# Performance work log

Hardware: AMD Instinct MI355X
Metric: run time of the kernel (lower is better)

The kernel has to match this reference:

```python
import jax, jax.numpy as jnp
import numpy as np

N = 100_000          # nodes
E = 3_200_000        # edges
DIM = 64             # filt_conv_dimension
L = 3                # filt_conv_number
MAX_DEG = 64         # embedding table size = MAX_DEG + 1
SUM_DIMS = DIM * (L + 1)  # 256, fc input
BN_EPS = 1e-5
NEG_SLOPE = 0.01


def _leaky(x):
    return jnp.where(x >= 0, x, NEG_SLOPE * x)


def _batchnorm(x, g, b):
    # training-mode BN over the node axis
    mu = jnp.mean(x, axis=0, keepdims=True)
    var = jnp.var(x, axis=0, keepdims=True)
    return g * (x - mu) * jax.lax.rsqrt(var + BN_EPS) + b


def setup_inputs() -> dict:
    key = jax.random.key(0)
    ks = jax.random.split(key, 16)
    s = 0.05
    inp = {
        "node_deg": jax.random.randint(ks[0], (N,), 0, MAX_DEG, dtype=jnp.int32),
        "edge_index": jax.random.randint(ks[1], (2, E), 0, N, dtype=jnp.int32),
        "embed_deg": jax.random.normal(ks[2], (MAX_DEG + 1, DIM), jnp.float32) * s,
        "eps": jnp.zeros((L,), jnp.float32),
        "W1": jax.random.normal(ks[3], (L, DIM, DIM), jnp.float32) * s,
        "b1": jnp.zeros((L, DIM), jnp.float32),
        "W2": jax.random.normal(ks[4], (L, DIM, DIM), jnp.float32) * s,
        "b2": jnp.zeros((L, DIM), jnp.float32),
        "bn_g": jnp.ones((L, DIM), jnp.float32),
        "bn_b": jnp.zeros((L, DIM), jnp.float32),
        "fc_W1": jax.random.normal(ks[5], (SUM_DIMS, DIM), jnp.float32) * s,
        "fc_b1": jnp.zeros((DIM,), jnp.float32),
        "fc_bn_g": jnp.ones((DIM,), jnp.float32),
        "fc_bn_b": jnp.zeros((DIM,), jnp.float32),
        "fc_W2": jax.random.normal(ks[6], (DIM, 1), jnp.float32) * s,
        "fc_b2": jnp.zeros((1,), jnp.float32),
    }
    return inp


def reference(node_deg, edge_index, embed_deg, eps, W1, b1, W2, b2,
              bn_g, bn_b, fc_W1, fc_b1, fc_bn_g, fc_bn_b, fc_W2, fc_b2):
    src, dst = edge_index[0], edge_index[1]
    h = embed_deg[node_deg]                       # [N, DIM]
    z = [h]
    for l in range(L):
        x = z[-1]
        # GINConv: (1+eps)*x_i + sum_{j->i} x_j, then MLP lin_lrelu_lin
        agg = jax.ops.segment_sum(x[src], dst, num_segments=N)  # [N, DIM]
        m = (1.0 + eps[l]) * x + agg
        h1 = _leaky(m @ W1[l] + b1[l])
        out = h1 @ W2[l] + b2[l]
        out = _leaky(_batchnorm(out, bn_g[l], bn_b[l]))
        z.append(out)
    xcat = jnp.concatenate(z, axis=1)             # [N, SUM_DIMS]
    hfc = _leaky(_batchnorm(xcat @ fc_W1 + fc_b1, fc_bn_g, fc_bn_b))
    ret = jax.nn.sigmoid(hfc @ fc_W2 + fc_b2)     # [N, 1]
    return jnp.squeeze(ret, axis=-1)              # [N]
```

## Files before the change

### kernel.cpp

```cpp
#include <hip/hip_runtime.h>
#include <hip/hip_bf16.h>

#define NN 100000
#define NE 3200000
#define D 64
#define BN_EPS 1e-5f

#define NP 512
#define CHUNK 6250
#define NB 391
#define SPREAD 16

typedef float v2f __attribute__((ext_vector_type(2)));

#define FMA4(accr, xs, w4) \
  accr.x += (xs) * (w4).x; accr.y += (xs) * (w4).y; \
  accr.z += (xs) * (w4).z; accr.w += (xs) * (w4).w;

__global__ __launch_bounds__(256) void bucket_kernel(const int* __restrict__ ei,
    const int* __restrict__ deg, int* __restrict__ rec, int* __restrict__ S) {
  __shared__ int cntL[392];
  __shared__ int curL[392];
  __shared__ int scanbuf[256];
  int t = threadIdx.x;
  int p = blockIdx.x;
  int e0 = p * CHUNK;
  cntL[t] = 0;
  if (t < 136) cntL[256 + t] = 0;
  __syncthreads();
  {
    int e = t;
    for (; e + 768 < CHUNK; e += 1024) {
      int d0 = ei[NE + e0 + e];
      int d1 = ei[NE + e0 + e + 256];
      int d2 = ei[NE + e0 + e + 512];
      int d3 = ei[NE + e0 + e + 768];
      atomicAdd(&cntL[(unsigned)d0 >> 8], 1);
      atomicAdd(&cntL[(unsigned)d1 >> 8], 1);
      atomicAdd(&cntL[(unsigned)d2 >> 8], 1);
      atomicAdd(&cntL[(unsigned)d3 >> 8], 1);
    }
    for (; e < CHUNK; e += 256) {
      int dd = ei[NE + e0 + e];
      atomicAdd(&cntL[(unsigned)dd >> 8], 1);
    }
  }
  __syncthreads();
  int a0 = 0, a1 = 0;
  if (t < 196) { a0 = cntL[2 * t]; a1 = cntL[2 * t + 1]; }
  int s = a0 + a1;
  scanbuf[t] = s;
  __syncthreads();
  for (int off = 1; off < 256; off <<= 1) {
    int x = (t >= off) ? scanbuf[t - off] : 0;
    __syncthreads();
    scanbuf[t] += x;
    __syncthreads();
  }
  int ex = scanbuf[t] - s;
  if (t < 196) {
    curL[2 * t]     = ex;
    curL[2 * t + 1] = ex + a0;
    S[p * 392 + 2 * t]     = e0 + ex;
    S[p * 392 + 2 * t + 1] = e0 + ex + a0;
  }
  __syncthreads();
  {
    int e = t;
    for (; e + 768 < CHUNK; e += 1024) {
      int s0 = ei[e0 + e],       d0 = ei[NE + e0 + e];
      int s1 = ei[e0 + e + 256], d1 = ei[NE + e0 + e + 256];
      int s2 = ei[e0 + e + 512], d2 = ei[NE + e0 + e + 512];
      int s3 = ei[e0 + e + 768], d3 = ei[NE + e0 + e + 768];
      int g0 = deg[s0], g1 = deg[s1], g2 = deg[s2], g3 = deg[s3];
      int p0 = atomicAdd(&curL[(unsigned)d0 >> 8], 1);
      int p1 = atomicAdd(&curL[(unsigned)d1 >> 8], 1);
      int p2 = atomicAdd(&curL[(unsigned)d2 >> 8], 1);
      int p3 = atomicAdd(&curL[(unsigned)d3 >> 8], 1);
      rec[e0 + p0] = s0 | ((d0 & 255) << 17) | (g0 << 25);
      rec[e0 + p1] = s1 | ((d1 & 255) << 17) | (g1 << 25);
      rec[e0 + p2] = s2 | ((d2 & 255) << 17) | (g2 << 25);
      rec[e0 + p3] = s3 | ((d3 & 255) << 17) | (g3 << 25);
    }
    for (; e < CHUNK; e += 256) {
      int ss = ei[e0 + e];
      int dd = ei[NE + e0 + e];
      int dg = deg[ss];
      int b = (unsigned)dd >> 8;
      int pos = atomicAdd(&curL[b], 1);
      rec[e0 + pos] = ss | ((dd & 255) << 17) | (dg << 25);
    }
  }
}

__global__ __launch_bounds__(256) void bucketsum_kernel(const int* __restrict__ S,
    int* __restrict__ bsum) {
  __shared__ int sh[256];
  int B = blockIdx.x;
  int t = threadIdx.x;
  int c = 0;
  for (int p = t; p < NP; p += 256)
    c += S[p * 392 + B + 1] - S[p * 392 + B];
  sh[t] = c;
  __syncthreads();
  for (int o = 128; o > 0; o >>= 1) {
    if (t < o) sh[t] += sh[t + o];
    __syncthreads();
  }
  if (t == 0) bsum[B] = sh[0];
}

__global__ __launch_bounds__(512) void scan2_kernel(int* __restrict__ bsum) {
  __shared__ int sh[512];
  int t = threadIdx.x;
  int v = (t < NB) ? bsum[t] : 0;
  sh[t] = v;
  __syncthreads();
  for (int o = 1; o < 512; o <<= 1) {
    int x = (t >= o) ? sh[t - o] : 0;
    __syncthreads();
    sh[t] += x;
    __syncthreads();
  }
  if (t < NB) bsum[t] = sh[t] - v;
}

__global__ __launch_bounds__(512) void sort_kernel(const int* __restrict__ rec,
    const int* __restrict__ S, const int* __restrict__ bsum,
    int* __restrict__ csroff, int* __restrict__ csrsrc,
    unsigned* __restrict__ cnt8) {
  __shared__ int cntL[256];
  __shared__ int curL[256];
  __shared__ unsigned hist[256 * 33];
  int t = threadIdx.x;
  int B = blockIdx.x;
  if (t < 256) cntL[t] = 0;
  for (int k = t; k < 256 * 33; k += 512) hist[k] = 0;
  __syncthreads();
  int lane = t & 15;
  int g = t >> 4;
  for (int p = g; p < NP; p += 32) {
    int s0 = S[p * 392 + B], s1 = S[p * 392 + B + 1];
    for (int e = s0 + lane; e < s1; e += 16) {
      int r = rec[e];
      int dl = (r >> 17) & 255;
      int dg = (unsigned)r >> 25;
      atomicAdd(&cntL[dl], 1);
      atomicAdd(&hist[dl * 33 + (dg >> 1)], (dg & 1) ? 0x10000u : 1u);
    }
  }
  __syncthreads();
  int v = 0;
  if (t < 256) { v = cntL[t]; curL[t] = v; }
  __syncthreads();
  for (int o = 1; o < 256; o <<= 1) {
    int x = 0;
    if (t < 256 && t >= o) x = curL[t - o];
    __syncthreads();
    if (t < 256) curL[t] += x;
    __syncthreads();
  }
  int b0 = bsum[B];
  if (t < 256) {
    int excl = curL[t] - v;
    int node = B * 256 + t;
    if (node <= NN) csroff[node] = b0 + excl;
  }
  __syncthreads();
  if (t < 256) curL[t] = b0 + (curL[t] - v);
  if (t < 256) {
    int node = B * 256 + t;
    if (node < NN) {
      #pragma unroll
      for (int j = 0; j < 16; j++) {
        unsigned p0 = hist[t * 33 + 2 * j];
        unsigned p1 = hist[t * 33 + 2 * j + 1];
        unsigned p = (p0 & 255) | (((p0 >> 16) & 255) << 8)
                   | ((p1 & 255) << 16) | (((p1 >> 16) & 255) << 24);
        cnt8[(long)node * 16 + j] = p;
      }
    }
  }
  __syncthreads();
  for (int p = g; p < NP; p += 32) {
    int s0 = S[p * 392 + B], s1 = S[p * 392 + B + 1];
    for (int e = s0 + lane; e < s1; e += 16) {
      int r = rec[e];
      int pos = atomicAdd(&curL[(r >> 17) & 255], 1);
      csrsrc[pos] = r & 0x1FFFF;
    }
  }
}

__global__ __launch_bounds__(256) void agg_kernel(const int* __restrict__ off,
    const int* __restrict__ srcs, const unsigned* __restrict__ xh32,
    float* __restrict__ agg) {
  int t = threadIdx.x;
  int lane = t & 15;
  int g = t >> 4;
  int i = blockIdx.x * 16 + g;
  int e0 = off[i], e1 = off[i + 1];
  float s0 = 0.f, s1 = 0.f, s2 = 0.f, s3 = 0.f;
  int e = e0;
  for (; e + 4 <= e1; e += 4) {
    int j0 = srcs[e + 0], j1 = srcs[e + 1], j2 = srcs[e + 2], j3 = srcs[e + 3];
    unsigned u0 = xh32[(long)j0 * 16 + lane];
    unsigned u1 = xh32[(long)j1 * 16 + lane];
    unsigned u2 = xh32[(long)j2 * 16 + lane];
    unsigned u3 = xh32[(long)j3 * 16 + lane];
    v2f l0 = __builtin_amdgcn_cvt_pk_f32_fp8((int)u0, false);
    v2f h0 = __builtin_amdgcn_cvt_pk_f32_fp8((int)u0, true);
    v2f l1 = __builtin_amdgcn_cvt_pk_f32_fp8((int)u1, false);
    v2f h1 = __builtin_amdgcn_cvt_pk_f32_fp8((int)u1, true);
    v2f l2 = __builtin_amdgcn_cvt_pk_f32_fp8((int)u2, false);
    v2f h2 = __builtin_amdgcn_cvt_pk_f32_fp8((int)u2, true);
    v2f l3 = __builtin_amdgcn_cvt_pk_f32_fp8((int)u3, false);
    v2f h3 = __builtin_amdgcn_cvt_pk_f32_fp8((int)u3, true);
    s0 += (l0.x + l1.x) + (l2.x + l3.x);
    s1 += (l0.y + l1.y) + (l2.y + l3.y);
    s2 += (h0.x + h1.x) + (h2.x + h3.x);
    s3 += (h0.y + h1.y) + (h2.y + h3.y);
  }
  for (; e < e1; e++) {
    unsigned u = xh32[(long)srcs[e] * 16 + lane];
    v2f lo = __builtin_amdgcn_cvt_pk_f32_fp8((int)u, false);
    v2f hi = __builtin_amdgcn_cvt_pk_f32_fp8((int)u, true);
    s0 += lo.x; s1 += lo.y; s2 += hi.x; s3 += hi.y;
  }
  *(float4*)&agg[(long)i * D + lane * 4] = make_float4(s0, s1, s2, s3);
}

__global__ __launch_bounds__(256) void layer_kernel(
    const float* __restrict__ X,
    const float* __restrict__ AGG,
    const unsigned* __restrict__ CNT8, const float* __restrict__ EMB,
    const int* __restrict__ deg, float* __restrict__ Z0,
    const float* __restrict__ epsv, int l,
    const float* __restrict__ W1, const float* __restrict__ b1,
    const float* __restrict__ W2, const float* __restrict__ b2,
    float* __restrict__ Z, float* __restrict__ spread)
{
  __shared__ float Ws[64][64];
  __shared__ float XsT[64][64];
  int t = threadIdx.x;
  int i0 = blockIdx.x * 64;
  float alpha = 1.0f + epsv[l];
  int c0 = (t & 15) * 4;
  int r0 = (t >> 4) * 4;
  int wr = t >> 4;
  int wc = (t & 15) * 4;
  int row = t & 63;
  int gi_row = i0 + row;
  int gis_row = (gi_row < NN) ? gi_row : NN - 1;
  int kb = (t >> 6) * 16;

  if (CNT8) {
    #pragma unroll
    for (int j = 0; j < 4; j++)
      *(float4*)&Ws[wr + 16 * j][wc] = *(const float4*)&EMB[(long)(wr + 16 * j) * D + wc];
    #pragma unroll
    for (int j = 0; j < 4; j++) {
      unsigned u = CNT8[(long)gis_row * 16 + (kb >> 2) + j];
      int k = kb + 4 * j;
      XsT[k + 0][row] = (float)(u & 255);
      XsT[k + 1][row] = (float)((u >> 8) & 255);
      XsT[k + 2][row] = (float)((u >> 16) & 255);
      XsT[k + 3][row] = (float)(u >> 24);
    }
    __syncthreads();
    float4 acc[4];
    #pragma unroll
    for (int r = 0; r < 4; r++) acc[r] = make_float4(0.f, 0.f, 0.f, 0.f);
    #pragma unroll 8
    for (int k = 0; k < 64; k++) {
      float4 w4 = *(const float4*)&Ws[k][c0];
      float4 x4 = *(const float4*)&XsT[k][r0];
      FMA4(acc[0], x4.x, w4); FMA4(acc[1], x4.y, w4);
      FMA4(acc[2], x4.z, w4); FMA4(acc[3], x4.w, w4);
    }
    __syncthreads();
    #pragma unroll
    for (int r = 0; r < 4; r++) {
      int gi = i0 + r0 + r;
      int gis = (gi < NN) ? gi : NN - 1;
      float4 xv = *(const float4*)&EMB[(long)deg[gis] * D + c0];
      if (gi < NN) *(float4*)&Z0[(long)gi * 256 + c0] = xv;
      XsT[c0 + 0][r0 + r] = alpha * xv.x + acc[r].x;
      XsT[c0 + 1][r0 + r] = alpha * xv.y + acc[r].y;
      XsT[c0 + 2][r0 + r] = alpha * xv.z + acc[r].z;
      XsT[c0 + 3][r0 + r] = alpha * xv.w + acc[r].w;
    }
    #pragma unroll
    for (int j = 0; j < 4; j++)
      *(float4*)&Ws[wr + 16 * j][wc] = *(const float4*)&W1[(long)(wr + 16 * j) * D + wc];
    __syncthreads();
  } else {
    #pragma unroll
    for (int j = 0; j < 4; j++)
      *(float4*)&Ws[wr + 16 * j][wc] = *(const float4*)&W1[(long)(wr + 16 * j) * D + wc];
    #pragma unroll
    for (int j = 0; j < 4; j++) {
      int k = kb + 4 * j;
      float4 xv = *(const float4*)&X[(long)gis_row * 256 + k];
      float4 a4 = *(const float4*)&AGG[(long)gis_row * D + k];
      XsT[k + 0][row] = alpha * xv.x + a4.x;
      XsT[k + 1][row] = alpha * xv.y + a4.y;
      XsT[k + 2][row] = alpha * xv.z + a4.z;
      XsT[k + 3][row] = alpha * xv.w + a4.w;
    }
    __syncthreads();
  }

  float4 h[4];
  {
    float4 b4 = *(const float4*)&b1[c0];
    #pragma unroll
    for (int r = 0; r < 4; r++) h[r] = b4;
  }
  #pragma unroll 8
  for (int k = 0; k < 64; k++) {
    float4 w4 = *(const float4*)&Ws[k][c0];
    float4 x4 = *(const float4*)&XsT[k][r0];
    FMA4(h[0], x4.x, w4); FMA4(h[1], x4.y, w4);
    FMA4(h[2], x4.z, w4); FMA4(h[3], x4.w, w4);
  }
  #pragma unroll
  for (int r = 0; r < 4; r++) {
    h[r].x = (h[r].x >= 0.0f) ? h[r].x : 0.01f * h[r].x;
    h[r].y = (h[r].y >= 0.0f) ? h[r].y : 0.01f * h[r].y;
    h[r].z = (h[r].z >= 0.0f) ? h[r].z : 0.01f * h[r].z;
    h[r].w = (h[r].w >= 0.0f) ? h[r].w : 0.01f * h[r].w;
  }
  __syncthreads();
  #pragma unroll
  for (int r = 0; r < 4; r++) {
    XsT[c0 + 0][r0 + r] = h[r].x;
    XsT[c0 + 1][r0 + r] = h[r].y;
    XsT[c0 + 2][r0 + r] = h[r].z;
    XsT[c0 + 3][r0 + r] = h[r].w;
  }
  #pragma unroll
  for (int j = 0; j < 4; j++)
    *(float4*)&Ws[wr + 16 * j][wc] = *(const float4*)&W2[(long)(wr + 16 * j) * D + wc];
  __syncthreads();

  float4 z[4];
  {
    float4 b4 = *(const float4*)&b2[c0];
    #pragma unroll
    for (int r = 0; r < 4; r++) z[r] = b4;
  }
  #pragma unroll 8
  for (int k = 0; k < 64; k++) {
    float4 w4 = *(const float4*)&Ws[k][c0];
    float4 x4 = *(const float4*)&XsT[k][r0];
    FMA4(z[0], x4.x, w4); FMA4(z[1], x4.y, w4);
    FMA4(z[2], x4.z, w4); FMA4(z[3], x4.w, w4);
  }
  #pragma unroll
  for (int r = 0; r < 4; r++) {
    int gi = i0 + r0 + r;
    if (gi < NN) *(float4*)&Z[(long)gi * 256 + c0] = z[r];
  }

  float s[4] = {0, 0, 0, 0}, sq[4] = {0, 0, 0, 0};
  #pragma unroll
  for (int r = 0; r < 4; r++) {
    if (i0 + r0 + r < NN) {
      s[0] += z[r].x; sq[0] += z[r].x * z[r].x;
      s[1] += z[r].y; sq[1] += z[r].y * z[r].y;
      s[2] += z[r].z; sq[2] += z[r].z * z[r].z;
      s[3] += z[r].w; sq[3] += z[r].w * z[r].w;
    }
  }
  __syncthreads();
  float* red = &XsT[0][0];
  int grp = t >> 4;
  #pragma unroll
  for (int j = 0; j < 4; j++) {
    red[grp * 64 + c0 + j] = s[j];
    red[1024 + grp * 64 + c0 + j] = sq[j];
  }
  __syncthreads();
  if (t < 64) {
    float a = 0.0f, b = 0.0f;
    #pragma unroll
    for (int g = 0; g < 16; g++) {
      a += red[g * 64 + t];
      b += red[1024 + g * 64 + t];
    }
    int slot = blockIdx.x & (SPREAD - 1);
    atomicAdd(&spread[slot * 128 + t], a);
    atomicAdd(&spread[slot * 128 + 64 + t], b);
  }
}

__global__ __launch_bounds__(256) void fc1_kernel(
    const float* __restrict__ X,
    const float* __restrict__ W, const float* __restrict__ bias,
    float* __restrict__ Y, float* __restrict__ spread)
{
  __shared__ float Ws[64][64];
  __shared__ float XsT[64][64];
  int t = threadIdx.x;
  int i0 = blockIdx.x * 64;
  int c0 = (t & 15) * 4;
  int r0 = (t >> 4) * 4;
  int wr = t >> 4;
  int wc = (t & 15) * 4;

  float4 acc[4];
  {
    float4 b4 = *(const float4*)&bias[c0];
    #pragma unroll
    for (int r = 0; r < 4; r++) acc[r] = b4;
  }
  for (int kc = 0; kc < 256; kc += 64) {
    __syncthreads();
    #pragma unroll
    for (int j = 0; j < 4; j++)
      *(float4*)&Ws[wr + 16 * j][wc] = *(const float4*)&W[(long)(kc + wr + 16 * j) * D + wc];
    {
      int row = t & 63;
      int gi = i0 + row;
      int gis = (gi < NN) ? gi : NN - 1;
      int kb = (t >> 6) * 16;
      #pragma unroll
      for (int j = 0; j < 4; j++) {
        int k = kb + 4 * j;
        float4 xv = *(const float4*)&X[(long)gis * 256 + kc + k];
        XsT[k + 0][row] = xv.x;
        XsT[k + 1][row] = xv.y;
        XsT[k + 2][row] = xv.z;
        XsT[k + 3][row] = xv.w;
      }
    }
    __syncthreads();
    #pragma unroll 8
    for (int k = 0; k < 64; k++) {
      float4 w4 = *(const float4*)&Ws[k][c0];
      float4 x4 = *(const float4*)&XsT[k][r0];
      FMA4(acc[0], x4.x, w4); FMA4(acc[1], x4.y, w4);
      FMA4(acc[2], x4.z, w4); FMA4(acc[3], x4.w, w4);
    }
  }
  #pragma unroll
  for (int r = 0; r < 4; r++) {
    int gi = i0 + r0 + r;
    if (gi < NN) *(float4*)&Y[(long)gi * D + c0] = acc[r];
  }
  float s[4] = {0, 0, 0, 0}, sq[4] = {0, 0, 0, 0};
  #pragma unroll
  for (int r = 0; r < 4; r++) {
    if (i0 + r0 + r < NN) {
      s[0] += acc[r].x; sq[0] += acc[r].x * acc[r].x;
      s[1] += acc[r].y; sq[1] += acc[r].y * acc[r].y;
      s[2] += acc[r].z; sq[2] += acc[r].z * acc[r].z;
      s[3] += acc[r].w; sq[3] += acc[r].w * acc[r].w;
    }
  }
  __syncthreads();
  float* red = &XsT[0][0];
  int grp = t >> 4;
  #pragma unroll
  for (int j = 0; j < 4; j++) {
    red[grp * 64 + c0 + j] = s[j];
    red[1024 + grp * 64 + c0 + j] = sq[j];
  }
  __syncthreads();
  if (t < 64) {
    float a = 0.0f, b = 0.0f;
    #pragma unroll
    for (int g = 0; g < 16; g++) {
      a += red[g * 64 + t];
      b += red[1024 + g * 64 + t];
    }
    int slot = blockIdx.x & (SPREAD - 1);
    atomicAdd(&spread[slot * 128 + t], a);
    atomicAdd(&spread[slot * 128 + 64 + t], b);
  }
}

__global__ __launch_bounds__(256) void bn_apply_kernel(float* __restrict__ Zs,
    const float* __restrict__ spread,
    const float* __restrict__ g, const float* __restrict__ b,
    unsigned short* __restrict__ Outh) {
  __shared__ float st[128];
  int t = threadIdx.x;
  if (t < 128) {
    float a = 0.0f;
    #pragma unroll
    for (int gg = 0; gg < SPREAD; gg++) a += spread[gg * 128 + t];
    st[t] = a;
  }
  __syncthreads();
  int idx = blockIdx.x * 256 + t;
  int i = idx >> 5, dp = (idx & 31) * 2;
  if (i >= NN) return;
  float invn = 1.0f / (float)NN;
  float v0, v1;
  {
    float mu = st[dp] * invn;
    float var = fmaxf(st[64 + dp] * invn - mu * mu, 0.0f);
    float sc = g[dp] * rsqrtf(var + BN_EPS);
    v0 = sc * (Zs[(long)i * 256 + dp] - mu) + b[dp];
    v0 = (v0 >= 0.0f) ? v0 : 0.01f * v0;
  }
  {
    float mu = st[dp + 1] * invn;
    float var = fmaxf(st[64 + dp + 1] * invn - mu * mu, 0.0f);
    float sc = g[dp + 1] * rsqrtf(var + BN_EPS);
    v1 = sc * (Zs[(long)i * 256 + dp + 1] - mu) + b[dp + 1];
    v1 = (v1 >= 0.0f) ? v1 : 0.01f * v1;
  }
  Zs[(long)i * 256 + dp]     = v0;
  Zs[(long)i * 256 + dp + 1] = v1;
  if (Outh) {
    int packed = __builtin_amdgcn_cvt_pk_fp8_f32(v0, v1, 0, false);
    Outh[(long)i * 32 + (dp >> 1)] = (unsigned short)packed;
  }
}

__global__ __launch_bounds__(256) void fc2bn_kernel(const float* __restrict__ H,
    const float* __restrict__ spread,
    const float* __restrict__ g, const float* __restrict__ b,
    const float* __restrict__ W2, const float* __restrict__ b2,
    float* __restrict__ out) {
  __shared__ float st[128];
  int tid = threadIdx.x;
  if (tid < 128) {
    float a = 0.0f;
    #pragma unroll
    for (int gg = 0; gg < SPREAD; gg++) a += spread[gg * 128 + tid];
    st[tid] = a;
  }
  __syncthreads();
  int k = tid & 63, q = tid >> 6;
  int i = blockIdx.x * 4 + q;
  float invn = 1.0f / (float)NN;
  float mu = st[k] * invn;
  float var = fmaxf(st[64 + k] * invn - mu * mu, 0.0f);
  float sc = g[k] * rsqrtf(var + BN_EPS);
  float v = 0.0f;
  if (i < NN) {
    float hv = sc * (H[(long)i * D + k] - mu) + b[k];
    hv = (hv >= 0.0f) ? hv : 0.01f * hv;
    v = hv * W2[k];
  }
  #pragma unroll
  for (int off = 32; off > 0; off >>= 1)
    v += __shfl_down(v, off);
  if (k == 0 && i < NN) {
    float x = v + b2[0];
    out[i] = 1.0f / (1.0f + __expf(-x));
  }
}

extern "C" void kernel_launch(void* const* d_in, const int* in_sizes, int n_in,
                              void* d_out, int out_size, void* d_ws, size_t ws_size,
                              hipStream_t stream) {
  const int*   node_deg   = (const int*)d_in[0];
  const int*   edge_index = (const int*)d_in[1];
  const float* embedw     = (const float*)d_in[2];
  const float* eps        = (const float*)d_in[3];
  const float* W1         = (const float*)d_in[4];
  const float* b1         = (const float*)d_in[5];
  const float* W2         = (const float*)d_in[6];
  const float* b2         = (const float*)d_in[7];
  const float* bn_g       = (const float*)d_in[8];
  const float* bn_b       = (const float*)d_in[9];
  const float* fc_W1      = (const float*)d_in[10];
  const float* fc_b1      = (const float*)d_in[11];
  const float* fc_bn_g    = (const float*)d_in[12];
  const float* fc_bn_b    = (const float*)d_in[13];
  const float* fc_W2      = (const float*)d_in[14];
  const float* fc_b2      = (const float*)d_in[15];

  float* zcat   = (float*)d_ws;
  float* agg    = zcat + (long)NN * 256;
  float* statsS = agg + (long)NN * D;
  float* statsF = statsS + 4 * SPREAD * 128;
  int*   csroff = (int*)(statsF + 512);
  int*   bsum   = csroff + NN + 1;
  int*   csrsrc = bsum + 512;
  int*   rec    = csrsrc + NE;
  int*   S      = rec + NE;
  unsigned* cnt8 = (unsigned*)(S + NP * 392);
  unsigned short* xh = (unsigned short*)rec;

  const int rowBlocks   = NN / 4;
  const int layerBlocks = (NN + 63) / 64;
  const int aggBlocks   = NN / 16;
  const int bnBlocks    = (NN * 32 + 255) / 256;

  bucket_kernel<<<NP, 256, 0, stream>>>(edge_index, node_deg, rec, S);
  bucketsum_kernel<<<NB, 256, 0, stream>>>(S, bsum);
  scan2_kernel<<<1, 512, 0, stream>>>(bsum);
  sort_kernel<<<NB, 512, 0, stream>>>(rec, S, bsum, csroff, csrsrc, cnt8);

  hipMemsetAsync(statsS, 0, (size_t)(4 * SPREAD * 128) * sizeof(float), stream);

  for (int l = 0; l < 3; ++l) {
    if (l > 0)
      agg_kernel<<<aggBlocks, 256, 0, stream>>>(csroff, csrsrc,
          (const unsigned*)xh, agg);
    layer_kernel<<<layerBlocks, 256, 0, stream>>>(zcat + l * D,
        (l == 0) ? nullptr : agg,
        (l == 0) ? cnt8 : nullptr, embedw, node_deg, zcat,
        eps, l,
        W1 + (long)l * D * D, b1 + (long)l * D,
        W2 + (long)l * D * D, b2 + (long)l * D,
        zcat + (l + 1) * D, statsS + (long)l * SPREAD * 128);
    bn_apply_kernel<<<bnBlocks, 256, 0, stream>>>(zcat + (l + 1) * D,
        statsS + (long)l * SPREAD * 128,
        bn_g + (long)l * D, bn_b + (long)l * D,
        (l < 2) ? xh : nullptr);
  }

  fc1_kernel<<<layerBlocks, 256, 0, stream>>>(zcat, fc_W1, fc_b1, agg,
      statsS + 3L * SPREAD * 128);
  fc2bn_kernel<<<rowBlocks, 256, 0, stream>>>(agg, statsS + 3L * SPREAD * 128,
      fc_bn_g, fc_bn_b, fc_W2, fc_b2, (float*)d_out);
}
```

Baseline: 519.9 us.

## Fuse CSR neighbor aggregation into layer kernel, dropping separate agg pass

Removes the standalone agg_kernel and performs the fp8 gather-sum over CSR neighbors inside layer_kernel for layers 1 and 2, writing the sums straight into the shared XsT tile. This avoids writing and re-reading the N×64 fp32 agg buffer and saves two kernel launches. In exchange, each 256-thread block now does the irregular gather for 64 rows (4 rows per 16-lane group in sequence) before its matmul. That lowers the parallelism available to hide latency and adds a barrier before the combine step.

```diff
diff --git a/kernel.cpp b/kernel.cpp
--- a/kernel.cpp
+++ b/kernel.cpp
@@ -192,47 +192,10 @@
   }
 }
 
-__global__ __launch_bounds__(256) void agg_kernel(const int* __restrict__ off,
-    const int* __restrict__ srcs, const unsigned* __restrict__ xh32,
-    float* __restrict__ agg) {
-  int t = threadIdx.x;
-  int lane = t & 15;
-  int g = t >> 4;
-  int i = blockIdx.x * 16 + g;
-  int e0 = off[i], e1 = off[i + 1];
-  float s0 = 0.f, s1 = 0.f, s2 = 0.f, s3 = 0.f;
-  int e = e0;
-  for (; e + 4 <= e1; e += 4) {
-    int j0 = srcs[e + 0], j1 = srcs[e + 1], j2 = srcs[e + 2], j3 = srcs[e + 3];
-    unsigned u0 = xh32[(long)j0 * 16 + lane];
-    unsigned u1 = xh32[(long)j1 * 16 + lane];
-    unsigned u2 = xh32[(long)j2 * 16 + lane];
-    unsigned u3 = xh32[(long)j3 * 16 + lane];
-    v2f l0 = __builtin_amdgcn_cvt_pk_f32_fp8((int)u0, false);
-    v2f h0 = __builtin_amdgcn_cvt_pk_f32_fp8((int)u0, true);
-    v2f l1 = __builtin_amdgcn_cvt_pk_f32_fp8((int)u1, false);
-    v2f h1 = __builtin_amdgcn_cvt_pk_f32_fp8((int)u1, true);
-    v2f l2 = __builtin_amdgcn_cvt_pk_f32_fp8((int)u2, false);
-    v2f h2 = __builtin_amdgcn_cvt_pk_f32_fp8((int)u2, true);
-    v2f l3 = __builtin_amdgcn_cvt_pk_f32_fp8((int)u3, false);
-    v2f h3 = __builtin_amdgcn_cvt_pk_f32_fp8((int)u3, true);
-    s0 += (l0.x + l1.x) + (l2.x + l3.x);
-    s1 += (l0.y + l1.y) + (l2.y + l3.y);
-    s2 += (h0.x + h1.x) + (h2.x + h3.x);
-    s3 += (h0.y + h1.y) + (h2.y + h3.y);
-  }
-  for (; e < e1; e++) {
-    unsigned u = xh32[(long)srcs[e] * 16 + lane];
-    v2f lo = __builtin_amdgcn_cvt_pk_f32_fp8((int)u, false);
-    v2f hi = __builtin_amdgcn_cvt_pk_f32_fp8((int)u, true);
-    s0 += lo.x; s1 += lo.y; s2 += hi.x; s3 += hi.y;
-  }
-  *(float4*)&agg[(long)i * D + lane * 4] = make_float4(s0, s1, s2, s3);
-}
-
 __global__ __launch_bounds__(256) void layer_kernel(
     const float* __restrict__ X,
-    const float* __restrict__ AGG,
+    const int* __restrict__ off, const int* __restrict__ srcs,
+    const unsigned* __restrict__ xh32,
     const unsigned* __restrict__ CNT8, const float* __restrict__ EMB,
     const int* __restrict__ deg, float* __restrict__ Z0,
     const float* __restrict__ epsv, int l,
@@ -298,15 +261,59 @@
     #pragma unroll
     for (int j = 0; j < 4; j++)
       *(float4*)&Ws[wr + 16 * j][wc] = *(const float4*)&W1[(long)(wr + 16 * j) * D + wc];
+    {
+      int lane = t & 15;
+      int grp = t >> 4;
+      #pragma unroll
+      for (int rr = 0; rr < 4; rr++) {
+        int r = grp * 4 + rr;
+        int i = i0 + r;
+        float s0 = 0.f, s1 = 0.f, s2 = 0.f, s3 = 0.f;
+        if (i < NN) {
+          int e0 = off[i], e1 = off[i + 1];
+          int e = e0;
+          for (; e + 4 <= e1; e += 4) {
+            int j0 = srcs[e + 0], j1 = srcs[e + 1];
+            int j2 = srcs[e + 2], j3 = srcs[e + 3];
+            unsigned u0 = xh32[(long)j0 * 16 + lane];
+            unsigned u1 = xh32[(long)j1 * 16 + lane];
+            unsigned u2 = xh32[(long)j2 * 16 + lane];
+            unsigned u3 = xh32[(long)j3 * 16 + lane];
+            v2f l0 = __builtin_amdgcn_cvt_pk_f32_fp8((int)u0, false);
+            v2f h0 = __builtin_amdgcn_cvt_pk_f32_fp8((int)u0, true);
+            v2f l1 = __builtin_amdgcn_cvt_pk_f32_fp8((int)u1, false);
+            v2f h1 = __builtin_amdgcn_cvt_pk_f32_fp8((int)u1, true);
+            v2f l2 = __builtin_amdgcn_cvt_pk_f32_fp8((int)u2, false);
+            v2f h2 = __builtin_amdgcn_cvt_pk_f32_fp8((int)u2, true);
+            v2f l3 = __builtin_amdgcn_cvt_pk_f32_fp8((int)u3, false);
+            v2f h3 = __builtin_amdgcn_cvt_pk_f32_fp8((int)u3, true);
+            s0 += (l0.x + l1.x) + (l2.x + l3.x);
+            s1 += (l0.y + l1.y) + (l2.y + l3.y);
+            s2 += (h0.x + h1.x) + (h2.x + h3.x);
+            s3 += (h0.y + h1.y) + (h2.y + h3.y);
+          }
+          for (; e < e1; e++) {
+            unsigned u = xh32[(long)srcs[e] * 16 + lane];
+            v2f lo = __builtin_amdgcn_cvt_pk_f32_fp8((int)u, false);
+            v2f hi = __builtin_amdgcn_cvt_pk_f32_fp8((int)u, true);
+            s0 += lo.x; s1 += lo.y; s2 += hi.x; s3 += hi.y;
+          }
+        }
+        XsT[4 * lane + 0][r] = s0;
+        XsT[4 * lane + 1][r] = s1;
+        XsT[4 * lane + 2][r] = s2;
+        XsT[4 * lane + 3][r] = s3;
+      }
+    }
+    __syncthreads();
     #pragma unroll
     for (int j = 0; j < 4; j++) {
       int k = kb + 4 * j;
       float4 xv = *(const float4*)&X[(long)gis_row * 256 + k];
-      float4 a4 = *(const float4*)&AGG[(long)gis_row * D + k];
-      XsT[k + 0][row] = alpha * xv.x + a4.x;
-      XsT[k + 1][row] = alpha * xv.y + a4.y;
-      XsT[k + 2][row] = alpha * xv.z + a4.z;
-      XsT[k + 3][row] = alpha * xv.w + a4.w;
+      XsT[k + 0][row] = alpha * xv.x + XsT[k + 0][row];
+      XsT[k + 1][row] = alpha * xv.y + XsT[k + 1][row];
+      XsT[k + 2][row] = alpha * xv.z + XsT[k + 2][row];
+      XsT[k + 3][row] = alpha * xv.w + XsT[k + 3][row];
     }
     __syncthreads();
   }
@@ -590,7 +597,6 @@
 
   const int rowBlocks   = NN / 4;
   const int layerBlocks = (NN + 63) / 64;
-  const int aggBlocks   = NN / 16;
   const int bnBlocks    = (NN * 32 + 255) / 256;
 
   bucket_kernel<<<NP, 256, 0, stream>>>(edge_index, node_deg, rec, S);
@@ -601,11 +607,8 @@
   hipMemsetAsync(statsS, 0, (size_t)(4 * SPREAD * 128) * sizeof(float), stream);
 
   for (int l = 0; l < 3; ++l) {
-    if (l > 0)
-      agg_kernel<<<aggBlocks, 256, 0, stream>>>(csroff, csrsrc,
-          (const unsigned*)xh, agg);
     layer_kernel<<<layerBlocks, 256, 0, stream>>>(zcat + l * D,
-        (l == 0) ? nullptr : agg,
+        csroff, csrsrc, (const unsigned*)xh,
         (l == 0) ? cnt8 : nullptr, embedw, node_deg, zcat,
         eps, l,
         W1 + (long)l * D * D, b1 + (long)l * D,
```

New measurement: 548.2 us. +5.4%, slower.
